# Optimization experiments

Measured on AMD Instinct MI355X. Metric: run time of the kernel, lower is better.

The kernel has to match this reference:

```python
import jax, jax.numpy as jnp
import numpy as np

NUM_IN, IN_DIM, NUM_OUT, OUT_DIM, NUM_ROUTING = 1152, 8, 10, 16, 3
BATCH = 256


def squash(v):
    # v: (..., d). scale = |v|^2/(1+|v|^2) * v/|v|
    sq = jnp.sum(v * v, axis=-1, keepdims=True)
    scale = sq / (1.0 + sq)
    return scale * v / jnp.sqrt(sq + 1e-8)


def setup_inputs() -> dict:
    key = jax.random.key(0)
    k1, k2 = jax.random.split(key)
    input_capsules = jax.random.normal(k1, (BATCH, NUM_IN, IN_DIM), dtype=jnp.float32)
    W = jax.random.normal(k2, (NUM_IN, IN_DIM, NUM_OUT, OUT_DIM), dtype=jnp.float32) * 0.01
    return {"input_capsules": input_capsules, "W": W}


def reference(input_capsules, W):
    # u_hat: (b, i, j, o) -- predictions from each input capsule i for output capsule j
    u_hat = jnp.einsum('bid,idjo->bijo', input_capsules, W)
    b = jnp.zeros(u_hat.shape[:3] + (1,), dtype=u_hat.dtype)  # (b, i, j, 1)
    v = None
    for it in range(NUM_ROUTING):
        c = jax.nn.softmax(b, axis=2)                 # coupling coeffs over output capsules j
        s = jnp.sum(c * u_hat, axis=1)                # (b, j, o)
        v = squash(s)                                 # (b, j, o)
        if it < NUM_ROUTING - 1:
            agreement = jnp.sum(u_hat * v[:, None, :, :], axis=-1, keepdims=True)
            b = b + agreement
    return v
```

## Files before the change

### kernel.cpp

```cpp
#include <hip/hip_runtime.h>


#define NUM_IN 1152
#define NUM_OUT 10
#define OUT_DIM 16
#define BATCH 256
#define SLOTS 160
#define ICH_BLK 16
#define NCHUNK (NUM_IN / ICH_BLK)
#define BPB 16
#define NBT (BATCH / BPB)
#define WROW 1280

typedef unsigned int __attribute__((address_space(1))) as1_uint;
typedef unsigned int __attribute__((address_space(3))) as3_uint;

__device__ __forceinline__ void gll16(const float* g, float* l) {
  __builtin_amdgcn_global_load_lds((const as1_uint*)g, (as3_uint*)l, 16, 0, 0);
}

__device__ __forceinline__ float rowsum8_hi(float x) {
  int v;
  v = __builtin_amdgcn_update_dpp(0, __float_as_int(x), 0x114, 0xF, 0xF, true);
  x += __int_as_float(v);
  v = __builtin_amdgcn_update_dpp(0, __float_as_int(x), 0x112, 0xF, 0xF, true);
  x += __int_as_float(v);
  v = __builtin_amdgcn_update_dpp(0, __float_as_int(x), 0x111, 0xF, 0xF, true);
  x += __int_as_float(v);
  return x;
}

__device__ __forceinline__ float rowsum16(float x) {
  int v;
  v = __builtin_amdgcn_update_dpp(0, __float_as_int(x), 0x128, 0xF, 0xF, true);
  x += __int_as_float(v);
  v = __builtin_amdgcn_update_dpp(0, __float_as_int(x), 0x124, 0xF, 0xF, true);
  x += __int_as_float(v);
  v = __builtin_amdgcn_update_dpp(0, __float_as_int(x), 0x122, 0xF, 0xF, true);
  x += __int_as_float(v);
  v = __builtin_amdgcn_update_dpp(0, __float_as_int(x), 0x121, 0xF, 0xF, true);
  x += __int_as_float(v);
  return x;
}

template <int PASS, int R, bool PART>
__device__ __forceinline__ void compute_round(
    const float* __restrict__ x, const float* __restrict__ v0p,
    const float* __restrict__ v1p, float* __restrict__ outp, const float* Wb,
    int i, int b0, int lbase, int vbase, size_t obase) {
  float xd[2][8];
#pragma unroll
  for (int bb = 0; bb < 2; ++bb) {
    const float* px = x + ((size_t)(b0 + bb) * NUM_IN + i) * 8;
    const float4 a = *reinterpret_cast<const float4*>(px);
    const float4 c = *reinterpret_cast<const float4*>(px + 4);
    xd[bb][0] = a.x; xd[bb][1] = a.y; xd[bb][2] = a.z; xd[bb][3] = a.w;
    xd[bb][4] = c.x; xd[bb][5] = c.y; xd[bb][6] = c.z; xd[bb][7] = c.w;
  }

  float u[2][5][4];
  float cw[2][5];

#pragma unroll
  for (int jl = 0; jl < 5; ++jl) {
    float ax0 = 0.f, ay0 = 0.f, az0 = 0.f, aw0 = 0.f;
    float ax1 = 0.f, ay1 = 0.f, az1 = 0.f, aw1 = 0.f;
#pragma unroll
    for (int d = 0; d < 8; ++d) {
      const float4 w =
          *reinterpret_cast<const float4*>(Wb + lbase + (d * 10 + jl) * 128);
      ax0 = fmaf(xd[0][d], w.x, ax0); ay0 = fmaf(xd[0][d], w.y, ay0);
      az0 = fmaf(xd[0][d], w.z, az0); aw0 = fmaf(xd[0][d], w.w, aw0);
      ax1 = fmaf(xd[1][d], w.x, ax1); ay1 = fmaf(xd[1][d], w.y, ay1);
      az1 = fmaf(xd[1][d], w.z, az1); aw1 = fmaf(xd[1][d], w.w, aw1);
    }
    u[0][jl][0] = ax0; u[0][jl][1] = ay0; u[0][jl][2] = az0; u[0][jl][3] = aw0;
    u[1][jl][0] = ax1; u[1][jl][1] = ay1; u[1][jl][2] = az1; u[1][jl][3] = aw1;
    if (PASS >= 1) {
#pragma unroll
      for (int bb = 0; bb < 2; ++bb) {
        const float4 p = *reinterpret_cast<const float4*>(
            v0p + (b0 + bb) * SLOTS + vbase + jl * 16);
        float lgv = u[bb][jl][0] * p.x + u[bb][jl][1] * p.y +
                    u[bb][jl][2] * p.z + u[bb][jl][3] * p.w;
        if (PASS == 2) {
          const float4 q = *reinterpret_cast<const float4*>(
              v1p + (b0 + bb) * SLOTS + vbase + jl * 16);
          lgv += u[bb][jl][0] * q.x + u[bb][jl][1] * q.y +
                 u[bb][jl][2] * q.z + u[bb][jl][3] * q.w;
        }
        cw[bb][jl] = lgv;
      }
    }
  }

  if (PASS == 0) {
#pragma unroll
    for (int bb = 0; bb < 2; ++bb)
#pragma unroll
      for (int jl = 0; jl < 5; ++jl) cw[bb][jl] = 0.1f;
  } else {
#pragma unroll
    for (int bb = 0; bb < 2; ++bb) {
#pragma unroll
      for (int jl = 0; jl < 5; ++jl) {
        float v = cw[bb][jl];
        v += __shfl_xor(v, 8);
        v += __shfl_xor(v, 16);
        cw[bb][jl] = v;
      }
      float m = cw[bb][0];
#pragma unroll
      for (int jl = 1; jl < 5; ++jl) m = fmaxf(m, cw[bb][jl]);
      m = fmaxf(m, __shfl_xor(m, 32));
      float z = 0.f;
#pragma unroll
      for (int jl = 0; jl < 5; ++jl) {
        cw[bb][jl] = __expf(cw[bb][jl] - m);
        z += cw[bb][jl];
      }
      z += __shfl_xor(z, 32);
      const float rz = 1.0f / z;
#pragma unroll
      for (int jl = 0; jl < 5; ++jl) cw[bb][jl] *= rz;
    }
  }

  const bool wr = ((threadIdx.x & 7) == 7);
#pragma unroll
  for (int jl = 0; jl < 5; ++jl) {
#pragma unroll
    for (int bb = 0; bb < 2; ++bb) {
      const float sx = rowsum8_hi(cw[bb][jl] * u[bb][jl][0]);
      const float sy = rowsum8_hi(cw[bb][jl] * u[bb][jl][1]);
      const float sz = rowsum8_hi(cw[bb][jl] * u[bb][jl][2]);
      const float sw = rowsum8_hi(cw[bb][jl] * u[bb][jl][3]);
      if (wr) {
        if (PART) {
          float4* q =
              reinterpret_cast<float4*>(outp + obase + bb * SLOTS + jl * 16);
          float4 f = {sx, sy, sz, sw};
          if (R == 1) {
            const float4 o = *q;
            f.x += o.x; f.y += o.y; f.z += o.z; f.w += o.w;
          }
          *q = f;
        } else {
          float* p = outp + obase + bb * SLOTS + jl * 16;
          atomicAdd(p + 0, sx); atomicAdd(p + 1, sy);
          atomicAdd(p + 2, sz); atomicAdd(p + 3, sw);
        }
      }
    }
  }
}

template <int PASS, bool PART>
__global__ __launch_bounds__(512, 2) void caps_pass(
    const float* __restrict__ x, const float* __restrict__ W,
    const float* __restrict__ v0, const float* __restrict__ v1,
    float* __restrict__ outp) {
  __shared__ float Ws[2][10240];

  const int t = threadIdx.x;
  const int ic = blockIdx.x % NCHUNK;
  const int bt = blockIdx.x / NCHUNK;
  const int i0 = ic * ICH_BLK;

  const float* wg = W + (size_t)i0 * WROW;
#pragma unroll
  for (int k = 0; k < 5; ++k) {
    const int p = t + k * 512;
    const int g = (p & 7) * 320 + (p >> 5) * 4 + ((p >> 3) & 3);
    gll16(wg + g * 4, &Ws[0][p * 4]);
  }
#pragma unroll
  for (int k = 0; k < 5; ++k) {
    const int p = t + k * 512;
    const int g = (p & 7) * 320 + (p >> 5) * 4 + ((p >> 3) & 3);
    gll16(wg + 8 * WROW + g * 4, &Ws[1][p * 4]);
  }

  const int lane = t & 63;
  const int wave = t >> 6;
  const int i_sub = lane & 7;
  const int oq = (lane >> 3) & 3;
  const int jg = lane >> 5;
  const int b0 = bt * BPB + wave * 2;
  const int lbase = jg * 640 + oq * 32 + i_sub * 4;
  const int vbase = jg * 80 + oq * 4;
  const size_t obase =
      ((PART ? (size_t)ic * BATCH : (size_t)0) + b0) * SLOTS + vbase;

  asm volatile("s_waitcnt vmcnt(5)" ::: "memory");
  __builtin_amdgcn_s_barrier();
  compute_round<PASS, 0, PART>(x, v0, v1, outp, &Ws[0][0], i0 + i_sub, b0,
                               lbase, vbase, obase);
  asm volatile("s_waitcnt vmcnt(0)" ::: "memory");
  __builtin_amdgcn_s_barrier();
  compute_round<PASS, 1, PART>(x, v0, v1, outp, &Ws[1][0], i0 + 8 + i_sub, b0,
                               lbase, vbase, obase);
}

__global__ __launch_bounds__(192) void caps_reduce_squash(
    const float* __restrict__ part, float* __restrict__ v_out) {
  const int b = blockIdx.x;
  const int t = threadIdx.x;
  if (t < SLOTS) {
    float sv = 0.0f;
#pragma unroll 8
    for (int ic = 0; ic < NCHUNK; ++ic)
      sv += part[((size_t)ic * BATCH + b) * SLOTS + t];
    const float sq = rowsum16(sv * sv);
    const float scale = sq / (1.0f + sq) * rsqrtf(sq + 1e-8f);
    v_out[(size_t)b * SLOTS + t] = sv * scale;
  }
}

__global__ __launch_bounds__(192) void caps_squash(const float* s_in,
                                                   float* v_out,
                                                   float* s_zero) {
  const int b = blockIdx.x;
  const int t = threadIdx.x;
  if (t < SLOTS) {
    const float sv = s_in[(size_t)b * SLOTS + t];
    const float sq = rowsum16(sv * sv);
    const float scale = sq / (1.0f + sq) * rsqrtf(sq + 1e-8f);
    v_out[(size_t)b * SLOTS + t] = sv * scale;
    if (s_zero) s_zero[(size_t)b * SLOTS + t] = 0.0f;
  }
}

extern "C" void kernel_launch(void* const* d_in, const int* in_sizes, int n_in,
                              void* d_out, int out_size, void* d_ws,
                              size_t ws_size, hipStream_t stream) {
  const float* x = (const float*)d_in[0];
  const float* W = (const float*)d_in[1];
  float* out = (float*)d_out;

  const size_t part_elems = (size_t)NCHUNK * BATCH * SLOTS;
  const size_t need = (part_elems + 2 * BATCH * SLOTS) * sizeof(float);
  const dim3 pg(NCHUNK * NBT);

  if (ws_size >= need) {
    float* part = (float*)d_ws;
    float* v0 = part + part_elems;
    float* v1 = v0 + BATCH * SLOTS;
    caps_pass<0, true><<<pg, 512, 0, stream>>>(x, W, nullptr, nullptr, part);
    caps_reduce_squash<<<BATCH, 192, 0, stream>>>(part, v0);
    caps_pass<1, true><<<pg, 512, 0, stream>>>(x, W, v0, nullptr, part);
    caps_reduce_squash<<<BATCH, 192, 0, stream>>>(part, v1);
    caps_pass<2, true><<<pg, 512, 0, stream>>>(x, W, v0, v1, part);
    caps_reduce_squash<<<BATCH, 192, 0, stream>>>(part, out);
  } else {
    float* s_buf = (float*)d_ws;
    float* v0 = s_buf + BATCH * SLOTS;
    float* v1 = v0 + BATCH * SLOTS;
    hipMemsetAsync(s_buf, 0, (size_t)BATCH * SLOTS * sizeof(float), stream);
    caps_pass<0, false><<<pg, 512, 0, stream>>>(x, W, nullptr, nullptr, s_buf);
    caps_squash<<<BATCH, 192, 0, stream>>>(s_buf, v0, s_buf);
    caps_pass<1, false><<<pg, 512, 0, stream>>>(x, W, v0, nullptr, s_buf);
    caps_squash<<<BATCH, 192, 0, stream>>>(s_buf, v1, s_buf);
    caps_pass<2, false><<<pg, 512, 0, stream>>>(x, W, v0, v1, s_buf);
    caps_squash<<<BATCH, 192, 0, stream>>>(s_buf, out, nullptr);
  }
}
```

Baseline: 231.9 us.

## Remap lane layout, prefetch x early, use DPP/permlane reductions, reorder partials

Lanes are remapped so the output-capsule group sits at lane bit 4 and the o-quad at bits 3 and 5. The LDS layout for W is rearranged to match, so each lane reads contiguous float4s indexed by lane. The agreement logit reduction now uses a DPP row_shr and a permlane32 swap instead of ds_bpermute shuffles, and the softmax cross-group exchange becomes an xor-16 shuffle. Input x loads for both rounds are hoisted ahead of the second W prefetch, so their latency overlaps the LDS fill. The partial-sum buffer is reordered to batch-major so the reduce kernel reads contiguously. The risks are a wrong mapping between lanes and the new LDS layout, and higher register pressure from holding the prefetched x values.

Measured after the change: 229.5 us. No clear change (-1.0%).

```diff
diff --git a/kernel.cpp b/kernel.cpp
--- a/kernel.cpp
+++ b/kernel.cpp
@@ -14,9 +14,21 @@
 
 typedef unsigned int __attribute__((address_space(1))) as1_uint;
 typedef unsigned int __attribute__((address_space(3))) as3_uint;
+typedef int v2i __attribute__((ext_vector_type(2)));
 
 __device__ __forceinline__ void gll16(const float* g, float* l) {
   __builtin_amdgcn_global_load_lds((const as1_uint*)g, (as3_uint*)l, 16, 0, 0);
+}
+
+__device__ __forceinline__ float xor8_sum(float x) {
+  int v = __builtin_amdgcn_update_dpp(0, __float_as_int(x), 0x128, 0xF, 0xF, true);
+  return x + __int_as_float(v);
+}
+
+__device__ __forceinline__ float xor32_sum(float x) {
+  v2i r = __builtin_amdgcn_permlane32_swap(__float_as_int(x),
+                                           __float_as_int(x), false, false);
+  return __int_as_float(r.x) + __int_as_float(r.y);
 }
 
 __device__ __forceinline__ float rowsum8_hi(float x) {
@@ -45,17 +57,19 @@
 
 template <int PASS, int R, bool PART>
 __device__ __forceinline__ void compute_round(
-    const float* __restrict__ x, const float* __restrict__ v0p,
+    const float4 xv[2][2], const float* __restrict__ v0p,
     const float* __restrict__ v1p, float* __restrict__ outp, const float* Wb,
-    int i, int b0, int lbase, int vbase, size_t obase) {
+    int b0, int lane, int vbase, size_t obase) {
+  constexpr size_t BBS = PART ? (size_t)(NCHUNK * SLOTS) : (size_t)SLOTS;
+  const float* wsl = Wb + lane * 4;
+
   float xd[2][8];
 #pragma unroll
   for (int bb = 0; bb < 2; ++bb) {
-    const float* px = x + ((size_t)(b0 + bb) * NUM_IN + i) * 8;
-    const float4 a = *reinterpret_cast<const float4*>(px);
-    const float4 c = *reinterpret_cast<const float4*>(px + 4);
-    xd[bb][0] = a.x; xd[bb][1] = a.y; xd[bb][2] = a.z; xd[bb][3] = a.w;
-    xd[bb][4] = c.x; xd[bb][5] = c.y; xd[bb][6] = c.z; xd[bb][7] = c.w;
+    xd[bb][0] = xv[bb][0].x; xd[bb][1] = xv[bb][0].y;
+    xd[bb][2] = xv[bb][0].z; xd[bb][3] = xv[bb][0].w;
+    xd[bb][4] = xv[bb][1].x; xd[bb][5] = xv[bb][1].y;
+    xd[bb][6] = xv[bb][1].z; xd[bb][7] = xv[bb][1].w;
   }
 
   float u[2][5][4];
@@ -68,7 +82,7 @@
 #pragma unroll
     for (int d = 0; d < 8; ++d) {
       const float4 w =
-          *reinterpret_cast<const float4*>(Wb + lbase + (d * 10 + jl) * 128);
+          *reinterpret_cast<const float4*>(wsl + (d * 5 + jl) * 256);
       ax0 = fmaf(xd[0][d], w.x, ax0); ay0 = fmaf(xd[0][d], w.y, ay0);
       az0 = fmaf(xd[0][d], w.z, az0); aw0 = fmaf(xd[0][d], w.w, aw0);
       ax1 = fmaf(xd[1][d], w.x, ax1); ay1 = fmaf(xd[1][d], w.y, ay1);
@@ -89,7 +103,7 @@
           lgv += u[bb][jl][0] * q.x + u[bb][jl][1] * q.y +
                  u[bb][jl][2] * q.z + u[bb][jl][3] * q.w;
         }
-        cw[bb][jl] = lgv;
+        cw[bb][jl] = xor32_sum(xor8_sum(lgv));
       }
     }
   }
@@ -102,31 +116,24 @@
   } else {
 #pragma unroll
     for (int bb = 0; bb < 2; ++bb) {
-#pragma unroll
-      for (int jl = 0; jl < 5; ++jl) {
-        float v = cw[bb][jl];
-        v += __shfl_xor(v, 8);
-        v += __shfl_xor(v, 16);
-        cw[bb][jl] = v;
-      }
       float m = cw[bb][0];
 #pragma unroll
       for (int jl = 1; jl < 5; ++jl) m = fmaxf(m, cw[bb][jl]);
-      m = fmaxf(m, __shfl_xor(m, 32));
+      m = fmaxf(m, __shfl_xor(m, 16));
       float z = 0.f;
 #pragma unroll
       for (int jl = 0; jl < 5; ++jl) {
         cw[bb][jl] = __expf(cw[bb][jl] - m);
         z += cw[bb][jl];
       }
-      z += __shfl_xor(z, 32);
+      z += __shfl_xor(z, 16);
       const float rz = 1.0f / z;
 #pragma unroll
       for (int jl = 0; jl < 5; ++jl) cw[bb][jl] *= rz;
     }
   }
 
-  const bool wr = ((threadIdx.x & 7) == 7);
+  const bool wr = ((lane & 7) == 7);
 #pragma unroll
   for (int jl = 0; jl < 5; ++jl) {
 #pragma unroll
@@ -138,7 +145,7 @@
       if (wr) {
         if (PART) {
           float4* q =
-              reinterpret_cast<float4*>(outp + obase + bb * SLOTS + jl * 16);
+              reinterpret_cast<float4*>(outp + obase + bb * BBS + jl * 16);
           float4 f = {sx, sy, sz, sw};
           if (R == 1) {
             const float4 o = *q;
@@ -146,7 +153,7 @@
           }
           *q = f;
         } else {
-          float* p = outp + obase + bb * SLOTS + jl * 16;
+          float* p = outp + obase + bb * BBS + jl * 16;
           atomicAdd(p + 0, sx); atomicAdd(p + 1, sy);
           atomicAdd(p + 2, sz); atomicAdd(p + 3, sw);
         }
@@ -167,39 +174,63 @@
   const int bt = blockIdx.x / NCHUNK;
   const int i0 = ic * ICH_BLK;
 
-  const float* wg = W + (size_t)i0 * WROW;
-#pragma unroll
-  for (int k = 0; k < 5; ++k) {
-    const int p = t + k * 512;
-    const int g = (p & 7) * 320 + (p >> 5) * 4 + ((p >> 3) & 3);
-    gll16(wg + g * 4, &Ws[0][p * 4]);
-  }
-#pragma unroll
-  for (int k = 0; k < 5; ++k) {
-    const int p = t + k * 512;
-    const int g = (p & 7) * 320 + (p >> 5) * 4 + ((p >> 3) & 3);
-    gll16(wg + 8 * WROW + g * 4, &Ws[1][p * 4]);
-  }
-
   const int lane = t & 63;
   const int wave = t >> 6;
   const int i_sub = lane & 7;
-  const int oq = (lane >> 3) & 3;
-  const int jg = lane >> 5;
+  const int oq = ((lane >> 3) & 1) | ((lane >> 4) & 2);
+  const int jg = (lane >> 4) & 1;
   const int b0 = bt * BPB + wave * 2;
-  const int lbase = jg * 640 + oq * 32 + i_sub * 4;
   const int vbase = jg * 80 + oq * 4;
+
+  const float* wg = W + (size_t)i0 * WROW;
+#pragma unroll
+  for (int k = 0; k < 5; ++k) {
+    const int p = t + k * 512;
+    const int lp = p & 63;
+    const int dj = p >> 6;
+    const int d = dj / 5, jl = dj % 5;
+    const int g = (lp & 7) * 320 + d * 40 + jl * 4 + ((lp >> 4) & 1) * 20 +
+                  ((lp >> 3) & 1) + ((lp >> 5) & 1) * 2;
+    gll16(wg + g * 4, &Ws[0][p * 4]);
+  }
+
+  float4 xv[2][2][2];
+#pragma unroll
+  for (int r = 0; r < 2; ++r)
+#pragma unroll
+    for (int bb = 0; bb < 2; ++bb) {
+      const float* px =
+          x + ((size_t)(b0 + bb) * NUM_IN + i0 + r * 8 + i_sub) * 8;
+      xv[r][bb][0] = *reinterpret_cast<const float4*>(px);
+      xv[r][bb][1] = *reinterpret_cast<const float4*>(px + 4);
+    }
+
+  __builtin_amdgcn_sched_barrier(0);
+
+#pragma unroll
+  for (int k = 0; k < 5; ++k) {
+    const int p = t + k * 512;
+    const int lp = p & 63;
+    const int dj = p >> 6;
+    const int d = dj / 5, jl = dj % 5;
+    const int g = (lp & 7) * 320 + d * 40 + jl * 4 + ((lp >> 4) & 1) * 20 +
+                  ((lp >> 3) & 1) + ((lp >> 5) & 1) * 2;
+    gll16(wg + 8 * WROW + g * 4, &Ws[1][p * 4]);
+  }
+  __builtin_amdgcn_sched_barrier(0);
+
   const size_t obase =
-      ((PART ? (size_t)ic * BATCH : (size_t)0) + b0) * SLOTS + vbase;
+      PART ? ((size_t)b0 * NCHUNK + ic) * SLOTS + vbase
+           : (size_t)b0 * SLOTS + vbase;
 
   asm volatile("s_waitcnt vmcnt(5)" ::: "memory");
   __builtin_amdgcn_s_barrier();
-  compute_round<PASS, 0, PART>(x, v0, v1, outp, &Ws[0][0], i0 + i_sub, b0,
-                               lbase, vbase, obase);
+  compute_round<PASS, 0, PART>(xv[0], v0, v1, outp, &Ws[0][0], b0, lane,
+                               vbase, obase);
   asm volatile("s_waitcnt vmcnt(0)" ::: "memory");
   __builtin_amdgcn_s_barrier();
-  compute_round<PASS, 1, PART>(x, v0, v1, outp, &Ws[1][0], i0 + 8 + i_sub, b0,
-                               lbase, vbase, obase);
+  compute_round<PASS, 1, PART>(xv[1], v0, v1, outp, &Ws[1][0], b0, lane,
+                               vbase, obase);
 }
 
 __global__ __launch_bounds__(192) void caps_reduce_squash(
@@ -207,10 +238,10 @@
   const int b = blockIdx.x;
   const int t = threadIdx.x;
   if (t < SLOTS) {
+    const float* pb = part + (size_t)b * NCHUNK * SLOTS + t;
     float sv = 0.0f;
 #pragma unroll 8
-    for (int ic = 0; ic < NCHUNK; ++ic)
-      sv += part[((size_t)ic * BATCH + b) * SLOTS + t];
+    for (int ic = 0; ic < NCHUNK; ++ic) sv += pb[ic * SLOTS];
     const float sq = rowsum16(sv * sv);
     const float scale = sq / (1.0f + sq) * rsqrtf(sq + 1e-8f);
     v_out[(size_t)b * SLOTS + t] = sv * scale;
```
